# Kernel optimization log

Measured on AMD Instinct MI355X. Metric: run time of the kernel, lower is better.

Reference implementation:

```python
import jax, jax.numpy as jnp
import numpy as np

N, F, T, B, E, G = 50000, 3, 32, 32, 100000, 64
R = 1.1

def setup_inputs() -> dict:
    key = jax.random.key(0)
    k1, k2, k3, k4 = jax.random.split(key, 4)
    x = jax.random.normal(k1, (N, F), dtype=jnp.float32)
    v = jax.random.uniform(k2, (F, T), dtype=jnp.float32) - 0.5  # torch.rand(...) - 0.5
    lin = jnp.linspace(-R, R, B, dtype=jnp.float32).reshape(B, 1, 1)
    edge_index = jax.random.randint(k3, (2, E), 0, N)
    batch = jnp.sort(jax.random.randint(k4, (N,), 0, G))  # sorted graph ids per node
    return {"x": x, "v": v, "lin": lin, "edge_index": edge_index,
            "batch": batch, "num_graphs": G}


def _compute_ecc(h, index, lin, dim_size):
    # h: (M, T) heights; lin: (B,1,1); broadcast sigmoid -> (B, M, T)
    ecc = jax.nn.sigmoid(200.0 * (lin - h))
    # segment-sum over the M axis per graph; torch's segment_coo(...).movedim(0,1)
    # yields (dim_size, B, T), which equals segment_sum over axis 0 of (M, B, T).
    return jax.ops.segment_sum(jnp.moveaxis(ecc, 1, 0), index, num_segments=dim_size)


def reference(x, v, lin, edge_index, batch, num_graphs):
    nh = x @ v                                   # (N, T) node heights
    eh = jnp.max(nh[edge_index], axis=0)         # (E, T) edge max-gather
    ect_nodes = _compute_ecc(nh, batch, lin, num_graphs)                     # (G, B, T)
    ect_edges = _compute_ecc(eh, batch[edge_index[0]], lin, num_graphs)      # (G, B, T)
    return ect_nodes - ect_edges
```

## Files before the change

### kernel.cpp

```cpp
#include <hip/hip_runtime.h>

#define WG 256
#define G64 64
#define SPLITS 16
#define SCALEI 1048576
#define ISCALE 9.5367431640625e-07f

__global__ __launch_bounds__(WG) void k_bucket(const int* __restrict__ edge,
                                               const int* __restrict__ batch,
                                               int2* __restrict__ bucket,
                                               int* __restrict__ cursor,
                                               int* __restrict__ node_off,
                                               float* __restrict__ out,
                                               int E, int N, int CAP) {
    __shared__ int lc[G64], lb[G64];
    int tid = threadIdx.x;
    int bid = blockIdx.x;
    if (tid < G64) lc[tid] = 0;

    if (bid < G64) {
        float4* o4 = (float4*)(out + ((size_t)bid << 10));
        o4[tid] = make_float4(0.f, 0.f, 0.f, 0.f);
    }
    __syncthreads();

    int e = bid * WG + tid;
    int g = 0, r = 0, s = 0, d = 0;
    if (e < E) {
        s = edge[e];
        d = edge[E + e];
        g = batch[s];
        r = atomicAdd(&lc[g], 1);
    }
    __syncthreads();
    if (tid < G64 && lc[tid]) lb[tid] = atomicAdd(&cursor[tid], lc[tid]);
    __syncthreads();
    if (e < E) {
        int pos = lb[g] + r;
        if (pos < CAP) bucket[(size_t)g * CAP + pos] = make_int2(s, d);
    }

    if (bid == 0 && tid <= G64) {
        int lo = 0, hi = N;
        while (lo < hi) {
            int mid = (lo + hi) >> 1;
            if (batch[mid] < tid) lo = mid + 1; else hi = mid;
        }
        node_off[tid] = lo;
    }
}

__global__ __launch_bounds__(WG) void k_acc(const float* __restrict__ x,
                                            const float* __restrict__ v,
                                            const int2* __restrict__ bucket,
                                            const float* __restrict__ lin,
                                            const int* __restrict__ cursor,
                                            const int* __restrict__ node_off,
                                            float* __restrict__ out, int CAP) {
    __shared__ int   hist[34 * 32];
    __shared__ float colf[32 * 32];
    int tid = threadIdx.x;
    for (int i = tid; i < 34 * 32; i += WG) hist[i] = 0;

    int g = blockIdx.x;
    int n0 = node_off[g], n1 = node_off[g + 1];
    int nn = n1 - n0;
    int ne = cursor[g]; if (ne > CAP) ne = CAP;
    int L = nn + ne;
    int ipc = (L + SPLITS - 1) / SPLITS;
    int lo = blockIdx.y * ipc;
    int hi = lo + ipc; if (hi > L) hi = L;

    int t = tid & 31, sub = tid >> 5;
    float v0 = v[t], v1 = v[32 + t], v2 = v[64 + t];

    float lin0 = lin[0];
    float dlin = lin[1] - lin[0];
    const float LOG2E = 1.4426950408889634f;
    float d2 = 200.f * dlin * LOG2E;
    float inv_dlin = 1.f / dlin;
    float fstep = exp2f(-d2);
    __syncthreads();

    int nhi = hi < nn ? hi : nn;
    for (int idx = lo + sub; idx < nhi; idx += 8) {
        const float* xr = x + (size_t)(n0 + idx) * 3;
        float h = xr[0] * v0 + xr[1] * v1 + xr[2] * v2;
        float bs = (h - lin0) * inv_dlin;
        float bF = floorf(bs);
        float e0 = exp2f((bs - bF) * d2);
        float s0 = __builtin_amdgcn_rcpf(1.f + e0);
        float s1 = __builtin_amdgcn_rcpf(fmaf(e0, fstep, 1.f));
        int q0 = (int)(s0 * (float)SCALEI);
        int q1 = (int)(s1 * (float)SCALEI);
        int ib = (int)bF;
        int i0 = min(33, max(0, ib));
        int i1 = min(33, max(0, ib + 1));
        int i2 = min(33, max(0, ib + 2));
        atomicAdd(&hist[i0 * 32 + t], q0);
        atomicAdd(&hist[i1 * 32 + t], q1 - q0);
        atomicAdd(&hist[i2 * 32 + t], SCALEI - q1);
    }

    int elo = lo > nn ? lo : nn;
    for (int idx = elo + sub; idx < hi; idx += 8) {
        int2 sd = bucket[(size_t)g * CAP + (idx - nn)];
        const float* xs = x + (size_t)sd.x * 3;
        const float* xd = x + (size_t)sd.y * 3;
        float hs = xs[0] * v0 + xs[1] * v1 + xs[2] * v2;
        float hd = xd[0] * v0 + xd[1] * v1 + xd[2] * v2;
        float h = fmaxf(hs, hd);
        float bs = (h - lin0) * inv_dlin;
        float bF = floorf(bs);
        float e0 = exp2f((bs - bF) * d2);
        float s0 = __builtin_amdgcn_rcpf(1.f + e0);
        float s1 = __builtin_amdgcn_rcpf(fmaf(e0, fstep, 1.f));
        int q0 = (int)(s0 * (float)SCALEI);
        int q1 = (int)(s1 * (float)SCALEI);
        int ib = (int)bF;
        int i0 = min(33, max(0, ib));
        int i1 = min(33, max(0, ib + 1));
        int i2 = min(33, max(0, ib + 2));
        atomicAdd(&hist[i0 * 32 + t], -q0);
        atomicAdd(&hist[i1 * 32 + t], q0 - q1);
        atomicAdd(&hist[i2 * 32 + t], q1 - SCALEI);
    }

    __syncthreads();
    if (tid < 32) {
        int run = 0;
#pragma unroll
        for (int b = 0; b < 32; ++b) {
            run += hist[b * 32 + tid];
            colf[b * 32 + tid] = (float)run * ISCALE;
        }
    }
    __syncthreads();
    for (int c = tid; c < 1024; c += WG)
        unsafeAtomicAdd(&out[((size_t)g << 10) + c], colf[c]);
}

extern "C" void kernel_launch(void* const* d_in, const int* in_sizes, int n_in,
                              void* d_out, int out_size, void* d_ws, size_t ws_size,
                              hipStream_t stream) {
    const float* x     = (const float*)d_in[0];
    const float* v     = (const float*)d_in[1];
    const float* lin   = (const float*)d_in[2];
    const int*   edge  = (const int*)d_in[3];
    const int*   batch = (const int*)d_in[4];
    int N = in_sizes[4];
    int E = in_sizes[3] / 2;

    float* out = (float*)d_out;

    int* cursor   = (int*)d_ws;
    int* node_off = cursor + G64;
    int2* bucket  = (int2*)((char*)d_ws + 1024);
    long long cap_ws = (long long)((ws_size - 1024) / ((size_t)G64 * sizeof(int2)));
    int CAP = (int)(cap_ws < (long long)E ? cap_ws : (long long)E);

    hipMemsetAsync(cursor, 0, G64 * sizeof(int), stream);

    k_bucket<<<(E + WG - 1) / WG, WG, 0, stream>>>(edge, batch, bucket, cursor,
                                                   node_off, out, E, N, CAP);
    dim3 grid(G64, SPLITS);
    k_acc<<<grid, WG, 0, stream>>>(x, v, bucket, lin, cursor, node_off, out, CAP);
}
```

Before: 90.81 us.

## Fuse bucketing and histogram accumulation into one cooperative kernel with grid syncs

Replaces the memset plus two kernel launches with a single cooperative kernel of 512 blocks. The kernel zeroes the output and cursors, syncs the grid, buckets edges while processing nodes, syncs again, then accumulates edges. This removes launch overhead and inter-kernel gaps and overlaps node work with the bucketing phase. In exchange it adds two grid-wide barriers, halves the splits per graph (less parallelism in the edge phase), and has each block loop serially over its edge chunk in the bucket phase.

```diff
diff --git a/kernel.cpp b/kernel.cpp
--- a/kernel.cpp
+++ b/kernel.cpp
@@ -1,90 +1,87 @@
 #include <hip/hip_runtime.h>
+#include <hip/hip_cooperative_groups.h>
+
+namespace cg = cooperative_groups;
 
 #define WG 256
 #define G64 64
-#define SPLITS 16
+#define SPLITS 8
+#define NBLK (G64 * SPLITS)
 #define SCALEI 1048576
 #define ISCALE 9.5367431640625e-07f
 
-__global__ __launch_bounds__(WG) void k_bucket(const int* __restrict__ edge,
-                                               const int* __restrict__ batch,
-                                               int2* __restrict__ bucket,
-                                               int* __restrict__ cursor,
-                                               int* __restrict__ node_off,
-                                               float* __restrict__ out,
-                                               int E, int N, int CAP) {
-    __shared__ int lc[G64], lb[G64];
+__global__ __launch_bounds__(WG) void k_fused(const float* __restrict__ x,
+                                              const float* __restrict__ v,
+                                              const float* __restrict__ lin,
+                                              const int* __restrict__ edge,
+                                              const int* __restrict__ batch,
+                                              int2* __restrict__ bucket,
+                                              int* __restrict__ cursor,
+                                              int* __restrict__ node_off,
+                                              float* __restrict__ out,
+                                              int E, int N, int CAP) {
+    __shared__ int   hist[34 * 32];
+    __shared__ float colf[32 * 32];
+    __shared__ int   lc[G64], lb[G64];
+
+    cg::grid_group grid = cg::this_grid();
     int tid = threadIdx.x;
     int bid = blockIdx.x;
-    if (tid < G64) lc[tid] = 0;
+    int flat = bid * WG + tid;
 
-    if (bid < G64) {
-        float4* o4 = (float4*)(out + ((size_t)bid << 10));
-        o4[tid] = make_float4(0.f, 0.f, 0.f, 0.f);
-    }
-    __syncthreads();
-
-    int e = bid * WG + tid;
-    int g = 0, r = 0, s = 0, d = 0;
-    if (e < E) {
-        s = edge[e];
-        d = edge[E + e];
-        g = batch[s];
-        r = atomicAdd(&lc[g], 1);
-    }
-    __syncthreads();
-    if (tid < G64 && lc[tid]) lb[tid] = atomicAdd(&cursor[tid], lc[tid]);
-    __syncthreads();
-    if (e < E) {
-        int pos = lb[g] + r;
-        if (pos < CAP) bucket[(size_t)g * CAP + pos] = make_int2(s, d);
-    }
-
-    if (bid == 0 && tid <= G64) {
+    for (int i = tid; i < 34 * 32; i += WG) hist[i] = 0;
+    if (flat < 16384) ((float4*)out)[flat] = make_float4(0.f, 0.f, 0.f, 0.f);
+    if (flat < G64) cursor[flat] = 0;
+    if (flat >= 16384 && flat < 16384 + G64 + 1) {
+        int val = flat - 16384;
         int lo = 0, hi = N;
         while (lo < hi) {
             int mid = (lo + hi) >> 1;
-            if (batch[mid] < tid) lo = mid + 1; else hi = mid;
+            if (batch[mid] < val) lo = mid + 1; else hi = mid;
         }
-        node_off[tid] = lo;
+        node_off[val] = lo;
     }
-}
+    grid.sync();
 
-__global__ __launch_bounds__(WG) void k_acc(const float* __restrict__ x,
-                                            const float* __restrict__ v,
-                                            const int2* __restrict__ bucket,
-                                            const float* __restrict__ lin,
-                                            const int* __restrict__ cursor,
-                                            const int* __restrict__ node_off,
-                                            float* __restrict__ out, int CAP) {
-    __shared__ int   hist[34 * 32];
-    __shared__ float colf[32 * 32];
-    int tid = threadIdx.x;
-    for (int i = tid; i < 34 * 32; i += WG) hist[i] = 0;
-
-    int g = blockIdx.x;
-    int n0 = node_off[g], n1 = node_off[g + 1];
-    int nn = n1 - n0;
-    int ne = cursor[g]; if (ne > CAP) ne = CAP;
-    int L = nn + ne;
-    int ipc = (L + SPLITS - 1) / SPLITS;
-    int lo = blockIdx.y * ipc;
-    int hi = lo + ipc; if (hi > L) hi = L;
-
+    int g = bid / SPLITS, split = bid % SPLITS;
     int t = tid & 31, sub = tid >> 5;
     float v0 = v[t], v1 = v[32 + t], v2 = v[64 + t];
-
     float lin0 = lin[0];
     float dlin = lin[1] - lin[0];
     const float LOG2E = 1.4426950408889634f;
     float d2 = 200.f * dlin * LOG2E;
     float inv_dlin = 1.f / dlin;
     float fstep = exp2f(-d2);
-    __syncthreads();
 
-    int nhi = hi < nn ? hi : nn;
-    for (int idx = lo + sub; idx < nhi; idx += 8) {
-        const float* xr = x + (size_t)(n0 + idx) * 3;
+    int c0 = (int)((long long)E * bid / NBLK);
+    int c1 = (int)((long long)E * (bid + 1) / NBLK);
+    for (int ts = c0; ts < c1; ts += WG) {
+        if (tid < G64) lc[tid] = 0;
+        __syncthreads();
+        int i = ts + tid;
+        int es = 0, ed = 0, eg = 0, er = 0, has = 0;
+        if (i < c1) {
+            es = edge[i];
+            ed = edge[E + i];
+            eg = batch[es];
+            er = atomicAdd(&lc[eg], 1);
+            has = 1;
+        }
+        __syncthreads();
+        if (tid < G64 && lc[tid]) lb[tid] = atomicAdd(&cursor[tid], lc[tid]);
+        __syncthreads();
+        if (has) {
+            int pos = lb[eg] + er;
+            if (pos < CAP) bucket[(size_t)eg * CAP + pos] = make_int2(es, ed);
+        }
+    }
+
+    int n0 = node_off[g], n1 = node_off[g + 1];
+    int nn = n1 - n0;
+    int a0 = n0 + (int)((long long)nn * split / SPLITS);
+    int a1 = n0 + (int)((long long)nn * (split + 1) / SPLITS);
+    for (int idx = a0 + sub; idx < a1; idx += 8) {
+        const float* xr = x + (size_t)idx * 3;
         float h = xr[0] * v0 + xr[1] * v1 + xr[2] * v2;
         float bs = (h - lin0) * inv_dlin;
         float bF = floorf(bs);
@@ -102,9 +99,14 @@
         atomicAdd(&hist[i2 * 32 + t], SCALEI - q1);
     }
 
-    int elo = lo > nn ? lo : nn;
-    for (int idx = elo + sub; idx < hi; idx += 8) {
-        int2 sd = bucket[(size_t)g * CAP + (idx - nn)];
+    grid.sync();
+
+    int ne = cursor[g]; if (ne > CAP) ne = CAP;
+    int ipc = (ne + SPLITS - 1) / SPLITS;
+    int lo = split * ipc;
+    int hi = lo + ipc; if (hi > ne) hi = ne;
+    for (int k = lo + sub; k < hi; k += 8) {
+        int2 sd = bucket[(size_t)g * CAP + k];
         const float* xs = x + (size_t)sd.x * 3;
         const float* xd = x + (size_t)sd.y * 3;
         float hs = xs[0] * v0 + xs[1] * v1 + xs[2] * v2;
@@ -150,6 +152,7 @@
     const int*   batch = (const int*)d_in[4];
     int N = in_sizes[4];
     int E = in_sizes[3] / 2;
+    (void)n_in; (void)out_size;
 
     float* out = (float*)d_out;
 
@@ -159,10 +162,8 @@
     long long cap_ws = (long long)((ws_size - 1024) / ((size_t)G64 * sizeof(int2)));
     int CAP = (int)(cap_ws < (long long)E ? cap_ws : (long long)E);
 
-    hipMemsetAsync(cursor, 0, G64 * sizeof(int), stream);
-
-    k_bucket<<<(E + WG - 1) / WG, WG, 0, stream>>>(edge, batch, bucket, cursor,
-                                                   node_off, out, E, N, CAP);
-    dim3 grid(G64, SPLITS);
-    k_acc<<<grid, WG, 0, stream>>>(x, v, bucket, lin, cursor, node_off, out, CAP);
+    void* args[] = {(void*)&x, (void*)&v, (void*)&lin, (void*)&edge, (void*)&batch,
+                    (void*)&bucket, (void*)&cursor, (void*)&node_off, (void*)&out,
+                    (void*)&E, (void*)&N, (void*)&CAP};
+    hipLaunchCooperativeKernel((void*)k_fused, dim3(NBLK), dim3(WG), args, 0, stream);
 }
```

New measurement: 205.2 us. 126% more time.
